# Performance work log

Measured on AMD Instinct MI355X. Metric: run time of the kernel, lower is better.

Reference implementation:

```python
import jax, jax.numpy as jnp
import numpy as np

DIM = 4096
N_HEADS = 32
HEAD_DIM = DIM // N_HEADS
BATCH = 2
SEQ = 1024
THETA = 10000.0
NEG_INF = -1e9


def _rope_cos_sin(seq_len, head_dim):
    # NOTE: original code constructs RotatePosEmbedding with config.dim but applies
    # it per-head; the only shape-consistent interpretation (standard Llama RoPE)
    # uses head_dim frequencies, which is what we implement.
    inv_freq = 1.0 / (THETA ** (jnp.arange(0, head_dim, 2, dtype=jnp.float32) / head_dim))
    angles = jnp.arange(seq_len, dtype=jnp.float32)[:, None] * inv_freq[None, :]  # [S, hd/2]
    return jnp.cos(angles), jnp.sin(angles)


def _apply_rope(x, cos, sin):
    # x: [B,S,H,hd]; rotate consecutive pairs (complex multiply)
    B, S, H, hd = x.shape
    xr = x.reshape(B, S, H, hd // 2, 2)
    x0, x1 = xr[..., 0], xr[..., 1]
    c = cos[None, :, None, :]
    s = sin[None, :, None, :]
    out = jnp.stack([x0 * c - x1 * s, x0 * s + x1 * c], axis=-1)
    return out.reshape(B, S, H, hd)


def setup_inputs() -> dict:
    key = jax.random.key(0)
    ks = jax.random.split(key, 9)
    x = jax.random.normal(ks[0], (BATCH, SEQ, DIM), dtype=jnp.float32)
    scale = 1.0 / np.sqrt(DIM)
    wq = jax.random.normal(ks[1], (DIM, DIM), dtype=jnp.float32) * scale
    wk = jax.random.normal(ks[2], (DIM, DIM), dtype=jnp.float32) * scale
    wv = jax.random.normal(ks[3], (DIM, DIM), dtype=jnp.float32) * scale
    wo = jax.random.normal(ks[4], (DIM, DIM), dtype=jnp.float32) * scale
    bq = jax.random.normal(ks[5], (DIM,), dtype=jnp.float32) * 0.01
    bk = jax.random.normal(ks[6], (DIM,), dtype=jnp.float32) * 0.01
    bv = jax.random.normal(ks[7], (DIM,), dtype=jnp.float32) * 0.01
    bo = jax.random.normal(ks[8], (DIM,), dtype=jnp.float32) * 0.01
    # causal additive mask [S,S]
    mask = jnp.where(jnp.tril(jnp.ones((SEQ, SEQ), dtype=bool)), 0.0, NEG_INF).astype(jnp.float32)
    return {"x": x, "wq": wq, "bq": bq, "wk": wk, "bk": bk, "wv": wv, "bv": bv,
            "wo": wo, "bo": bo, "mask": mask, "start_pos": 0}


def reference(x, wq, bq, wk, bk, wv, bv, wo, bo, mask, start_pos):
    B, S, D = x.shape
    H, hd = N_HEADS, D // N_HEADS
    q = (x @ wq.T + bq).reshape(B, S, H, hd)
    k = (x @ wk.T + bk).reshape(B, S, H, hd)
    v = (x @ wv.T + bv).reshape(B, S, H, hd)
    cos, sin = _rope_cos_sin(S, hd)
    q = _apply_rope(q, cos, sin)
    k = _apply_rope(k, cos, sin)
    # start_pos == 0 prefill: cache slice [:start_pos+S] equals current k/v
    scores = jnp.einsum('bqhd,bkhd->bhqk', q, k) / np.sqrt(hd).astype(np.float32)
    scores = scores + mask[None, None, :, :]
    attn = jax.nn.softmax(scores, axis=-1)
    out = jnp.einsum('bhqk,bkhd->bqhd', attn, v).reshape(B, S, D)
    return out @ wo.T + bo
```

## Files before the change

kernel.cpp:

```cpp
#include <hip/hip_runtime.h>
#include <hip/hip_bf16.h>

#define DIM   4096
#define NH    32
#define HD    128
#define BATCH 2
#define SEQ   1024
#define MROWS (BATCH*SEQ)
#define LDQ   12288

typedef __attribute__((ext_vector_type(8))) short bf16x8;
typedef __attribute__((ext_vector_type(4))) short s16x4;
typedef __attribute__((ext_vector_type(4))) float f32x4;

__device__ inline void gload_lds16(const void* g, void* l) {
  __builtin_amdgcn_global_load_lds(
      (const __attribute__((address_space(1))) void*)g,
      (__attribute__((address_space(3))) void*)l, 16, 0, 0);
}

__device__ inline float bf2f(short b) {
  unsigned u = ((unsigned)(unsigned short)b) << 16;
  return __uint_as_float(u);
}
__device__ inline unsigned short f2bfu(float f) {
  __hip_bfloat16 h = __float2bfloat16(f);
  return *reinterpret_cast<unsigned short*>(&h);
}

template <int N> __device__ __forceinline__ void wait_vm() {
  if constexpr (N == 0)      asm volatile("s_waitcnt vmcnt(0)" ::: "memory");
  else if constexpr (N == 7) asm volatile("s_waitcnt vmcnt(7)" ::: "memory");
  else                       asm volatile("s_waitcnt vmcnt(8)" ::: "memory");
}

__global__ void cvt_bf16_kernel(const float* __restrict__ in,
                                unsigned short* __restrict__ out, long n4) {
  long i = blockIdx.x * (long)blockDim.x + threadIdx.x;
  long stride = (long)gridDim.x * blockDim.x;
  for (; i < n4; i += stride) {
    float4 v = ((const float4*)in)[i];
    ushort4 o;
    o.x = f2bfu(v.x); o.y = f2bfu(v.y); o.z = f2bfu(v.z); o.w = f2bfu(v.w);
    ((ushort4*)out)[i] = o;
  }
}

__global__ void concat3_kernel(const float* __restrict__ a, const float* __restrict__ b,
                               const float* __restrict__ c, float* __restrict__ o) {
  int i = blockIdx.x * blockDim.x + threadIdx.x;
  if (i < 4096) o[i] = a[i];
  else if (i < 8192) o[i] = b[i - 4096];
  else if (i < 12288) o[i] = c[i - 8192];
}

__global__ void rope_table_kernel(float* __restrict__ cosT, float* __restrict__ sinT) {
  int s = blockIdx.x;
  int p = threadIdx.x;
  float inv = powf(10000.0f, -((float)(2 * p)) / 128.0f);
  float a = (float)s * inv;
  cosT[s * 64 + p] = cosf(a);
  sinT[s * 64 + p] = sinf(a);
}

__global__ void reduce_bias_kernel(const float* __restrict__ part,
                                   const float* __restrict__ bias,
                                   float* __restrict__ out) {
  long i = blockIdx.x * (long)blockDim.x + threadIdx.x;
  if (i >= (long)MROWS * DIM / 4) return;
  float4 a = ((const float4*)part)[i];
  float4 b = ((const float4*)(part + (size_t)MROWS * DIM))[i];
  float4 bb = ((const float4*)bias)[(int)(i & (DIM / 4 - 1))];
  float4 o;
  o.x = a.x + b.x + bb.x; o.y = a.y + b.y + bb.y;
  o.z = a.z + b.z + bb.z; o.w = a.w + b.w + bb.w;
  ((float4*)out)[i] = o;
}

template <typename OutT, bool QKV_MODE, int NB>
__global__ __launch_bounds__(512, 2) void gemm_q_kernel(
    const unsigned short* __restrict__ A, const unsigned short* __restrict__ Bw,
    const float* __restrict__ bias, OutT* __restrict__ C,
    int M, int N, int Kstr, int Klen,
    const float* __restrict__ cosT, const float* __restrict__ sinT) {
  constexpr int CBF = NB / 64;
  constexpr int BL  = NB / 64;
  constexpr int VM  = 4 + BL;
  constexpr int WNC = NB / 4;
  __shared__ unsigned short As[2][256 * 64];
  __shared__ unsigned short Bs[2][NB * 64];
  const int t = threadIdx.x;
  const int lane = t & 63;
  const int w = t >> 6;
  const int wm = w >> 2, wn = w & 3;
  const int np = lane & 15, hq = lane >> 4;

  int bid = blockIdx.y * gridDim.x + blockIdx.x;
  int nwg = gridDim.x * gridDim.y;
  int sb = (bid & 7) * (nwg >> 3) + (bid >> 3);
  int bx = sb % gridDim.x, by = sb / gridDim.x;
  const int m0 = by * 256, n0 = bx * NB;
  const int kb0 = blockIdx.z * Klen;
  const int NT = Klen >> 6;
  OutT* Cz = C + (size_t)blockIdx.z * M * N;

  auto stageA2 = [&](unsigned short* Asl, int kcol0, int j0) {
#pragma unroll
    for (int j = j0; j < j0 + 2; ++j) {
      int ci = j * 512 + t;
      int r = ci >> 3, c = ci & 7;
      gload_lds16(A + (size_t)(m0 + r) * Kstr + kcol0 + ((c ^ (r & 7)) << 3), Asl + ci * 8);
    }
  };
  auto stageB = [&](unsigned short* Bsl, int kcol0) {
#pragma unroll
    for (int j = 0; j < BL; ++j) {
      int ci = j * 512 + t;
      int r = ci >> 3, c = ci & 7;
      gload_lds16(Bw + (size_t)(n0 + r) * Kstr + kcol0 + ((c ^ (r & 7)) << 3), Bsl + ci * 8);
    }
  };

  stageA2(As[0], kb0, 0); stageA2(As[0], kb0, 2); stageB(Bs[0], kb0);
  stageA2(As[1], kb0 + 64, 0); stageA2(As[1], kb0 + 64, 2); stageB(Bs[1], kb0 + 64);

  f32x4 acc[8][CBF] = {};

  wait_vm<VM>();
  __builtin_amdgcn_s_barrier();

  int cur = 0;
#pragma unroll 1
  for (int kt = 0; kt < NT; ++kt) {
    const unsigned short* Asl = As[cur];
    const unsigned short* Bsl = Bs[cur];
    const int swz = np & 7;
    const int kn = kb0 + ((kt + 2) << 6);
    const bool more = (kt + 2 < NT);
    bf16x8 al[4][2], ah[4][2], bf[CBF][2];

#pragma unroll
    for (int rb = 0; rb < 4; ++rb)
#pragma unroll
      for (int kh = 0; kh < 2; ++kh)
        al[rb][kh] = *(const bf16x8*)&Asl[(wm * 128 + rb * 16 + np) * 64 +
                                          (((kh * 4 + hq) ^ swz) << 3)];
#pragma unroll
    for (int cb = 0; cb < CBF; ++cb)
#pragma unroll
      for (int kh = 0; kh < 2; ++kh)
        bf[cb][kh] = *(const bf16x8*)&Bsl[(wn * WNC + cb * 16 + np) * 64 +
                                          (((kh * 4 + hq) ^ swz) << 3)];
    __builtin_amdgcn_s_barrier();
    __builtin_amdgcn_s_setprio(1);
#pragma unroll
    for (int i = 0; i < 4; ++i)
#pragma unroll
      for (int j = 0; j < 2; ++j) {
        acc[i][j] = __builtin_amdgcn_mfma_f32_16x16x32_bf16(al[i][0], bf[j][0], acc[i][j], 0, 0, 0);
        acc[i][j] = __builtin_amdgcn_mfma_f32_16x16x32_bf16(al[i][1], bf[j][1], acc[i][j], 0, 0, 0);
      }
    __builtin_amdgcn_s_setprio(0);

#pragma unroll
    for (int rb = 0; rb < 4; ++rb)
#pragma unroll
      for (int kh = 0; kh < 2; ++kh)
        ah[rb][kh] = *(const bf16x8*)&Asl[(wm * 128 + 64 + rb * 16 + np) * 64 +
                                          (((kh * 4 + hq) ^ swz) << 3)];
    asm volatile("s_waitcnt lgkmcnt(0)" ::: "memory");
    __builtin_amdgcn_sched_barrier(0);
    __builtin_amdgcn_s_barrier();
    if (more) stageA2(As[cur], kn, 0);
    __builtin_amdgcn_s_setprio(1);
#pragma unroll
    for (int i = 0; i < 4; ++i)
#pragma unroll
      for (int j = 2; j < CBF; ++j) {
        acc[i][j] = __builtin_amdgcn_mfma_f32_16x16x32_bf16(al[i][0], bf[j][0], acc[i][j], 0, 0, 0);
        acc[i][j] = __builtin_amdgcn_mfma_f32_16x16x32_bf16(al[i][1], bf[j][1], acc[i][j], 0, 0, 0);
      }
    __builtin_amdgcn_s_setprio(0);
    __builtin_amdgcn_s_barrier();

    if (more) stageA2(As[cur], kn, 2);
    __builtin_amdgcn_s_setprio(1);
#pragma unroll
    for (int i = 0; i < 4; ++i)
#pragma unroll
      for (int j = 0; j < 2; ++j) {
        acc[i + 4][j] = __builtin_amdgcn_mfma_f32_16x16x32_bf16(ah[i][0], bf[j][0], acc[i + 4][j], 0, 0, 0);
        acc[i + 4][j] = __builtin_amdgcn_mfma_f32_16x16x32_bf16(ah[i][1], bf[j][1], acc[i + 4][j], 0, 0, 0);
      }
    __builtin_amdgcn_s_setprio(0);
    __builtin_amdgcn_s_barrier();

    if (more) stageB(Bs[cur], kn);
    __builtin_amdgcn_s_setprio(1);
#pragma unroll
    for (int i = 0; i < 4; ++i)
#pragma unroll
      for (int j = 2; j < CBF; ++j) {
        acc[i + 4][j] = __builtin_amdgcn_mfma_f32_16x16x32_bf16(ah[i][0], bf[j][0], acc[i + 4][j], 0, 0, 0);
        acc[i + 4][j] = __builtin_amdgcn_mfma_f32_16x16x32_bf16(ah[i][1], bf[j][1], acc[i + 4][j], 0, 0, 0);
      }
    __builtin_amdgcn_s_setprio(0);
    if (more) wait_vm<VM>();
    else      wait_vm<0>();
    __builtin_amdgcn_s_barrier();
    cur ^= 1;
  }

  const int orow0 = m0 + wm * 128;
  const int ocol0 = n0 + wn * WNC + np;
#pragma unroll
  for (int j = 0; j < CBF; ++j) {
    const int col = ocol0 + j * 16;
    float bj = QKV_MODE ? bias[col] : 0.0f;
    const int p0 = (col & 127) >> 1;
    const bool even = (lane & 1) == 0;
    const bool do_rope = QKV_MODE && (col < 8192);
#pragma unroll
    for (int i = 0; i < 8; ++i) {
#pragma unroll
      for (int r = 0; r < 4; ++r) {
        int orow = orow0 + i * 16 + hq * 4 + r;
        float v = acc[i][j][r] + bj;
        float pv = __shfl_xor(v, 1);
        if (do_rope) {
          int srow = orow & (SEQ - 1);
          float c = cosT[srow * 64 + p0];
          float s = sinT[srow * 64 + p0];
          v = even ? (v * c - pv * s) : (pv * s + v * c);
        }
        size_t off = (size_t)orow * N + col;
        if constexpr (sizeof(OutT) == 2)
          ((unsigned short*)Cz)[off] = f2bfu(v);
        else
          ((float*)Cz)[off] = v;
      }
    }
  }
}

__global__ __launch_bounds__(256, 1) void flash_attn_kernel(
    const unsigned short* __restrict__ QKV, unsigned short* __restrict__ O) {
  __shared__ unsigned short Ks[64 * 128];
  __shared__ unsigned short Vt[128 * 64];
  __shared__ unsigned short Ps[4][32 * 64];

  const int p  = blockIdx.x;
  const int bh = blockIdx.y;
  const int b  = bh >> 5;
  const int hh = bh & 31;
  const int t    = threadIdx.x;
  const int lane = t & 63;
  const int w    = t >> 6;
  const int np   = lane & 15;
  const int hq   = lane >> 4;

  const size_t rowbase = (size_t)b * SEQ * LDQ;
  const unsigned short* Qg = QKV + rowbase + (size_t)hh * HD;
  const unsigned short* Kg = QKV + rowbase + 4096 + (size_t)hh * HD;
  const unsigned short* Vg = QKV + rowbase + 8192 + (size_t)hh * HD;
  unsigned short* Og = O + (size_t)b * SEQ * DIM + (size_t)hh * HD;

  const int krow = t >> 2;
  const int kc0  = (t & 3) * 32;
  const int vr0  = (t & 15) * 4;
  const int vc0  = (t >> 4) * 8;

  unsigned short* Pw = &Ps[w][0];
  const float SCALE = 0.08838834764831843f;

  bf16x8 vk[4], vv[4];

#pragma unroll 1
  for (int pass = 0; pass < 2; ++pass) {
    const int qt    = pass ? (7 - p) : p;
    const int nt    = 2 * qt + 2;
    const int qbase = qt * 128 + w * 32;

    bf16x8 qf[2][4];
#pragma unroll
    for (int rb = 0; rb < 2; ++rb)
#pragma unroll
      for (int kb = 0; kb < 4; ++kb)
        qf[rb][kb] = *(const bf16x8*)&Qg[(size_t)(qbase + rb * 16 + np) * LDQ + kb * 32 + hq * 8];

    f32x4 acc[2][8] = {};
    float m_run[2][4], l_run[2][4];
#pragma unroll
    for (int rb = 0; rb < 2; ++rb)
#pragma unroll
      for (int r = 0; r < 4; ++r) { m_run[rb][r] = -3.0e38f; l_run[rb][r] = 0.0f; }

    {
      const unsigned short* kp = Kg + (size_t)krow * LDQ + kc0;
      const unsigned short* vp = Vg + (size_t)vr0 * LDQ + vc0;
#pragma unroll
      for (int jj = 0; jj < 4; ++jj) vk[jj] = *(const bf16x8*)(kp + jj * 8);
#pragma unroll
      for (int jj = 0; jj < 4; ++jj) vv[jj] = *(const bf16x8*)(vp + (size_t)jj * LDQ);
    }

#pragma unroll 1
    for (int kt = 0; kt < nt; ++kt) {
      __syncthreads();

#pragma unroll
      for (int jj = 0; jj < 4; ++jj) {
        int c = (t & 3) * 4 + jj;
        *(bf16x8*)((char*)Ks + krow * 256 + ((c ^ (krow & 7)) << 4)) = vk[jj];
      }
#pragma unroll
      for (int i = 0; i < 8; ++i) {
        int col = vc0 + i;
        s16x4 sv;
        sv[0] = vv[0][i]; sv[1] = vv[1][i]; sv[2] = vv[2][i]; sv[3] = vv[3][i];
        *(s16x4*)((char*)Vt + ((col * 128 + vr0 * 2) ^ ((col & 7) << 4))) = sv;
      }
      __syncthreads();

      if (kt + 1 < nt) {
        const unsigned short* kp = Kg + (size_t)((kt + 1) * 64 + krow) * LDQ + kc0;
        const unsigned short* vp = Vg + (size_t)((kt + 1) * 64 + vr0) * LDQ + vc0;
#pragma unroll
        for (int jj = 0; jj < 4; ++jj) vk[jj] = *(const bf16x8*)(kp + jj * 8);
#pragma unroll
        for (int jj = 0; jj < 4; ++jj) vv[jj] = *(const bf16x8*)(vp + (size_t)jj * LDQ);
      }

      f32x4 sc[4][2] = {};
#pragma unroll
      for (int ct = 0; ct < 4; ++ct) {
#pragma unroll
        for (int kb = 0; kb < 4; ++kb) {
          bf16x8 kf = *(const bf16x8*)((char*)Ks + (ct * 16 + np) * 256 +
                                       (((kb * 4 + hq) ^ (np & 7)) << 4));
          sc[ct][0] = __builtin_amdgcn_mfma_f32_16x16x32_bf16(qf[0][kb], kf, sc[ct][0], 0, 0, 0);
          sc[ct][1] = __builtin_amdgcn_mfma_f32_16x16x32_bf16(qf[1][kb], kf, sc[ct][1], 0, 0, 0);
        }
      }

      const bool maskt = (kt >= 2 * qt);
#pragma unroll
      for (int ct = 0; ct < 4; ++ct) {
        int kvc = kt * 64 + ct * 16 + np;
#pragma unroll
        for (int rb = 0; rb < 2; ++rb)
#pragma unroll
          for (int r = 0; r < 4; ++r) {
            float v = sc[ct][rb][r] * SCALE;
            if (maskt && kvc > qbase + rb * 16 + hq * 4 + r) v = -1.0e9f;
            sc[ct][rb][r] = v;
          }
      }

      float sf[2][4];
#pragma unroll
      for (int rb = 0; rb < 2; ++rb)
#pragma unroll
        for (int r = 0; r < 4; ++r) {
          float tmax = fmaxf(fmaxf(sc[0][rb][r], sc[1][rb][r]),
                             fmaxf(sc[2][rb][r], sc[3][rb][r]));
          tmax = fmaxf(tmax, __shfl_xor(tmax, 1));
          tmax = fmaxf(tmax, __shfl_xor(tmax, 2));
          tmax = fmaxf(tmax, __shfl_xor(tmax, 4));
          tmax = fmaxf(tmax, __shfl_xor(tmax, 8));
          float mn = fmaxf(m_run[rb][r], tmax);
          sf[rb][r] = __expf(m_run[rb][r] - mn);
          m_run[rb][r] = mn;
        }

#pragma unroll
      for (int rb = 0; rb < 2; ++rb)
#pragma unroll
        for (int r = 0; r < 4; ++r) {
          int prow = rb * 16 + hq * 4 + r;
          int swz = (prow & 7) << 4;
          float rsum = 0.f;
#pragma unroll
          for (int ct = 0; ct < 4; ++ct) {
            float pv = __expf(sc[ct][rb][r] - m_run[rb][r]);
            rsum += pv;
            *(unsigned short*)((char*)Pw + ((prow * 128 + (ct * 16 + np) * 2) ^ swz)) = f2bfu(pv);
          }
          rsum += __shfl_xor(rsum, 1);
          rsum += __shfl_xor(rsum, 2);
          rsum += __shfl_xor(rsum, 4);
          rsum += __shfl_xor(rsum, 8);
          l_run[rb][r] = l_run[rb][r] * sf[rb][r] + rsum;
        }

#pragma unroll
      for (int rb = 0; rb < 2; ++rb)
#pragma unroll
        for (int nt2 = 0; nt2 < 8; ++nt2)
#pragma unroll
          for (int r = 0; r < 4; ++r)
            acc[rb][nt2][r] *= sf[rb][r];

#pragma unroll
      for (int kb2 = 0; kb2 < 2; ++kb2) {
        bf16x8 pa0 = *(const bf16x8*)((char*)Pw +
            (((0 * 16 + np) * 128 + kb2 * 64 + hq * 16) ^ ((np & 7) << 4)));
        bf16x8 pa1 = *(const bf16x8*)((char*)Pw +
            (((1 * 16 + np) * 128 + kb2 * 64 + hq * 16) ^ ((np & 7) << 4)));
#pragma unroll
        for (int nt2 = 0; nt2 < 8; ++nt2) {
          int col = nt2 * 16 + np;
          bf16x8 vf = *(const bf16x8*)((char*)Vt +
              ((col * 128 + kb2 * 64 + hq * 16) ^ ((col & 7) << 4)));
          acc[0][nt2] = __builtin_amdgcn_mfma_f32_16x16x32_bf16(pa0, vf, acc[0][nt2], 0, 0, 0);
          acc[1][nt2] = __builtin_amdgcn_mfma_f32_16x16x32_bf16(pa1, vf, acc[1][nt2], 0, 0, 0);
        }
      }
    }

#pragma unroll
    for (int rb = 0; rb < 2; ++rb)
#pragma unroll
      for (int r = 0; r < 4; ++r) {
        float rl = 1.0f / l_run[rb][r];
        int orow = qbase + rb * 16 + hq * 4 + r;
#pragma unroll
        for (int nt2 = 0; nt2 < 8; ++nt2)
          Og[(size_t)orow * DIM + nt2 * 16 + np] = f2bfu(acc[rb][nt2][r] * rl);
      }
  }
}

extern "C" void kernel_launch(void* const* d_in, const int* in_sizes, int n_in,
                              void* d_out, int out_size, void* d_ws, size_t ws_size,
                              hipStream_t stream) {
  const float* x  = (const float*)d_in[0];
  const float* wq = (const float*)d_in[1];
  const float* bq = (const float*)d_in[2];
  const float* wk = (const float*)d_in[3];
  const float* bk = (const float*)d_in[4];
  const float* wv = (const float*)d_in[5];
  const float* bv = (const float*)d_in[6];
  const float* wo = (const float*)d_in[7];
  const float* bo = (const float*)d_in[8];
  float* out = (float*)d_out;

  char* ws = (char*)d_ws;
  unsigned short* wqkvb = (unsigned short*)(ws);
  float* part           = (float*)(ws);
  unsigned short* wob   = (unsigned short*)(ws + (96ll  << 20));
  unsigned short* xb    = (unsigned short*)(ws + (128ll << 20));
  unsigned short* qkv   = (unsigned short*)(ws + (144ll << 20));
  unsigned short* ab    = (unsigned short*)(ws + (192ll << 20));
  float* biasqkv = (float*)(ws + (208ll << 20));
  float* cosT    = (float*)(ws + (208ll << 20) + (64  << 10));
  float* sinT    = (float*)(ws + (208ll << 20) + (320 << 10));

  cvt_bf16_kernel<<<2048, 256, 0, stream>>>(x,  xb, (long)MROWS * DIM / 4);
  cvt_bf16_kernel<<<2048, 256, 0, stream>>>(wq, wqkvb,                        (long)DIM * DIM / 4);
  cvt_bf16_kernel<<<2048, 256, 0, stream>>>(wk, wqkvb + (size_t)DIM * DIM,    (long)DIM * DIM / 4);
  cvt_bf16_kernel<<<2048, 256, 0, stream>>>(wv, wqkvb + 2 * (size_t)DIM * DIM,(long)DIM * DIM / 4);
  cvt_bf16_kernel<<<2048, 256, 0, stream>>>(wo, wob, (long)DIM * DIM / 4);

  concat3_kernel<<<48, 256, 0, stream>>>(bq, bk, bv, biasqkv);
  rope_table_kernel<<<SEQ, 64, 0, stream>>>(cosT, sinT);

  dim3 gq(LDQ / 192, MROWS / 256, 1);
  gemm_q_kernel<unsigned short, true, 192><<<gq, 512, 0, stream>>>(
      xb, wqkvb, biasqkv, qkv, MROWS, LDQ, DIM, DIM, cosT, sinT);

  dim3 ga(4, BATCH * NH);
  flash_attn_kernel<<<ga, 256, 0, stream>>>(qkv, ab);

  dim3 go(DIM / 256, MROWS / 256, 2);
  gemm_q_kernel<float, false, 256><<<go, 512, 0, stream>>>(
      ab, wob, nullptr, part, MROWS, DIM, DIM, DIM / 2, nullptr, nullptr);

  reduce_bias_kernel<<<(MROWS * DIM / 4 + 255) / 256, 256, 0, stream>>>(part, bo, out);
}
```

Baseline: 529.2 us.

## Rewrite GEMM as 4-stage K=32 pipeline with fixed 256x256 tiles

Replaces the double-buffered K=64 GEMM, which interleaved partial stage loads between MFMA chunks under several barriers, with a four-slot ring of K=32 LDS buffers. Loads run three tiles ahead and each iteration needs only one barrier. The QKV GEMM now uses 256-wide N tiles instead of 192, giving 48x8 blocks. The aim is to cut barrier count and hide global-load latency better, at the cost of more iterations, a new swizzle, and fewer QKV workgroups.

```diff
diff --git a/kernel.cpp b/kernel.cpp
--- a/kernel.cpp
+++ b/kernel.cpp
@@ -30,7 +30,7 @@
 
 template <int N> __device__ __forceinline__ void wait_vm() {
   if constexpr (N == 0)      asm volatile("s_waitcnt vmcnt(0)" ::: "memory");
-  else if constexpr (N == 7) asm volatile("s_waitcnt vmcnt(7)" ::: "memory");
+  else if constexpr (N == 4) asm volatile("s_waitcnt vmcnt(4)" ::: "memory");
   else                       asm volatile("s_waitcnt vmcnt(8)" ::: "memory");
 }
 
@@ -77,18 +77,14 @@
   ((float4*)out)[i] = o;
 }
 
-template <typename OutT, bool QKV_MODE, int NB>
-__global__ __launch_bounds__(512, 2) void gemm_q_kernel(
+template <typename OutT, bool QKV_MODE>
+__global__ __launch_bounds__(512, 2) void gemm_v3_kernel(
     const unsigned short* __restrict__ A, const unsigned short* __restrict__ Bw,
     const float* __restrict__ bias, OutT* __restrict__ C,
     int M, int N, int Kstr, int Klen,
     const float* __restrict__ cosT, const float* __restrict__ sinT) {
-  constexpr int CBF = NB / 64;
-  constexpr int BL  = NB / 64;
-  constexpr int VM  = 4 + BL;
-  constexpr int WNC = NB / 4;
-  __shared__ unsigned short As[2][256 * 64];
-  __shared__ unsigned short Bs[2][NB * 64];
+  __shared__ unsigned short As[4][256 * 32];
+  __shared__ unsigned short Bs[4][256 * 32];
   const int t = threadIdx.x;
   const int lane = t & 63;
   const int w = t >> 6;
@@ -99,122 +95,77 @@
   int nwg = gridDim.x * gridDim.y;
   int sb = (bid & 7) * (nwg >> 3) + (bid >> 3);
   int bx = sb % gridDim.x, by = sb / gridDim.x;
-  const int m0 = by * 256, n0 = bx * NB;
+  const int m0 = by * 256, n0 = bx * 256;
   const int kb0 = blockIdx.z * Klen;
-  const int NT = Klen >> 6;
-  OutT* Cz = C + (size_t)blockIdx.z * M * N;
-
-  auto stageA2 = [&](unsigned short* Asl, int kcol0, int j0) {
-#pragma unroll
-    for (int j = j0; j < j0 + 2; ++j) {
+  const int NT = Klen >> 5;
+  OutT* Cz = C + (size_t)blockIdx.z * (size_t)M * N;
+
+  auto stage = [&](int slot, int kcol0) {
+#pragma unroll
+    for (int j = 0; j < 2; ++j) {
       int ci = j * 512 + t;
-      int r = ci >> 3, c = ci & 7;
-      gload_lds16(A + (size_t)(m0 + r) * Kstr + kcol0 + ((c ^ (r & 7)) << 3), Asl + ci * 8);
+      int r = ci >> 2, cg = (ci & 3) ^ ((r >> 1) & 3);
+      gload_lds16(A + (size_t)(m0 + r) * Kstr + kcol0 + cg * 8, &As[slot][ci * 8]);
+    }
+#pragma unroll
+    for (int j = 0; j < 2; ++j) {
+      int ci = j * 512 + t;
+      int r = ci >> 2, cg = (ci & 3) ^ ((r >> 1) & 3);
+      gload_lds16(Bw + (size_t)(n0 + r) * Kstr + kcol0 + cg * 8, &Bs[slot][ci * 8]);
     }
   };
-  auto stageB = [&](unsigned short* Bsl, int kcol0) {
-#pragma unroll
-    for (int j = 0; j < BL; ++j) {
-      int ci = j * 512 + t;
-      int r = ci >> 3, c = ci & 7;
-      gload_lds16(Bw + (size_t)(n0 + r) * Kstr + kcol0 + ((c ^ (r & 7)) << 3), Bsl + ci * 8);
-    }
-  };
-
-  stageA2(As[0], kb0, 0); stageA2(As[0], kb0, 2); stageB(Bs[0], kb0);
-  stageA2(As[1], kb0 + 64, 0); stageA2(As[1], kb0 + 64, 2); stageB(Bs[1], kb0 + 64);
-
-  f32x4 acc[8][CBF] = {};
-
-  wait_vm<VM>();
+
+  stage(0, kb0); stage(1, kb0 + 32); stage(2, kb0 + 64);
+
+  f32x4 acc[8][4] = {};
+
+  wait_vm<8>();
   __builtin_amdgcn_s_barrier();
 
-  int cur = 0;
 #pragma unroll 1
-  for (int kt = 0; kt < NT; ++kt) {
-    const unsigned short* Asl = As[cur];
-    const unsigned short* Bsl = Bs[cur];
-    const int swz = np & 7;
-    const int kn = kb0 + ((kt + 2) << 6);
-    const bool more = (kt + 2 < NT);
-    bf16x8 al[4][2], ah[4][2], bf[CBF][2];
-
-#pragma unroll
-    for (int rb = 0; rb < 4; ++rb)
-#pragma unroll
-      for (int kh = 0; kh < 2; ++kh)
-        al[rb][kh] = *(const bf16x8*)&Asl[(wm * 128 + rb * 16 + np) * 64 +
-                                          (((kh * 4 + hq) ^ swz) << 3)];
-#pragma unroll
-    for (int cb = 0; cb < CBF; ++cb)
-#pragma unroll
-      for (int kh = 0; kh < 2; ++kh)
-        bf[cb][kh] = *(const bf16x8*)&Bsl[(wn * WNC + cb * 16 + np) * 64 +
-                                          (((kh * 4 + hq) ^ swz) << 3)];
+  for (int u = 0; u < NT; ++u) {
+    const unsigned short* Asl = As[u & 3];
+    const unsigned short* Bsl = Bs[u & 3];
+    const int cswz = (np >> 1) & 3;
+    const int kc = (hq ^ cswz) << 3;
+    bf16x8 af[8], bf[4];
+#pragma unroll
+    for (int i = 0; i < 4; ++i)
+      af[i] = *(const bf16x8*)&Asl[(wm * 128 + i * 16 + np) * 32 + kc];
+#pragma unroll
+    for (int j = 0; j < 4; ++j)
+      bf[j] = *(const bf16x8*)&Bsl[(wn * 64 + j * 16 + np) * 32 + kc];
+#pragma unroll
+    for (int i = 4; i < 8; ++i)
+      af[i] = *(const bf16x8*)&Asl[(wm * 128 + i * 16 + np) * 32 + kc];
+
+    if (u + 3 < NT) stage((u + 3) & 3, kb0 + ((u + 3) << 5));
+
+    __builtin_amdgcn_s_setprio(1);
+#pragma unroll
+    for (int i = 0; i < 4; ++i)
+#pragma unroll
+      for (int j = 0; j < 4; ++j)
+        acc[i][j] = __builtin_amdgcn_mfma_f32_16x16x32_bf16(af[i], bf[j], acc[i][j], 0, 0, 0);
+    __builtin_amdgcn_s_setprio(0);
+    __builtin_amdgcn_s_setprio(1);
+#pragma unroll
+    for (int i = 4; i < 8; ++i)
+#pragma unroll
+      for (int j = 0; j < 4; ++j)
+        acc[i][j] = __builtin_amdgcn_mfma_f32_16x16x32_bf16(af[i], bf[j], acc[i][j], 0, 0, 0);
+    __builtin_amdgcn_s_setprio(0);
+
+    if (u + 3 < NT)      wait_vm<8>();
+    else if (u + 2 < NT) wait_vm<4>();
+    else                 wait_vm<0>();
     __builtin_amdgcn_s_barrier();
-    __builtin_amdgcn_s_setprio(1);
-#pragma unroll
-    for (int i = 0; i < 4; ++i)
-#pragma unroll
-      for (int j = 0; j < 2; ++j) {
-        acc[i][j] = __builtin_amdgcn_mfma_f32_16x16x32_bf16(al[i][0], bf[j][0], acc[i][j], 0, 0, 0);
-        acc[i][j] = __builtin_amdgcn_mfma_f32_16x16x32_bf16(al[i][1], bf[j][1], acc[i][j], 0, 0, 0);
-      }
-    __builtin_amdgcn_s_setprio(0);
-
-#pragma unroll
-    for (int rb = 0; rb < 4; ++rb)
-#pragma unroll
-      for (int kh = 0; kh < 2; ++kh)
-        ah[rb][kh] = *(const bf16x8*)&Asl[(wm * 128 + 64 + rb * 16 + np) * 64 +
-                                          (((kh * 4 + hq) ^ swz) << 3)];
-    asm volatile("s_waitcnt lgkmcnt(0)" ::: "memory");
-    __builtin_amdgcn_sched_barrier(0);
-    __builtin_amdgcn_s_barrier();
-    if (more) stageA2(As[cur], kn, 0);
-    __builtin_amdgcn_s_setprio(1);
-#pragma unroll
-    for (int i = 0; i < 4; ++i)
-#pragma unroll
-      for (int j = 2; j < CBF; ++j) {
-        acc[i][j] = __builtin_amdgcn_mfma_f32_16x16x32_bf16(al[i][0], bf[j][0], acc[i][j], 0, 0, 0);
-        acc[i][j] = __builtin_amdgcn_mfma_f32_16x16x32_bf16(al[i][1], bf[j][1], acc[i][j], 0, 0, 0);
-      }
-    __builtin_amdgcn_s_setprio(0);
-    __builtin_amdgcn_s_barrier();
-
-    if (more) stageA2(As[cur], kn, 2);
-    __builtin_amdgcn_s_setprio(1);
-#pragma unroll
-    for (int i = 0; i < 4; ++i)
-#pragma unroll
-      for (int j = 0; j < 2; ++j) {
-        acc[i + 4][j] = __builtin_amdgcn_mfma_f32_16x16x32_bf16(ah[i][0], bf[j][0], acc[i + 4][j], 0, 0, 0);
-        acc[i + 4][j] = __builtin_amdgcn_mfma_f32_16x16x32_bf16(ah[i][1], bf[j][1], acc[i + 4][j], 0, 0, 0);
-      }
-    __builtin_amdgcn_s_setprio(0);
-    __builtin_amdgcn_s_barrier();
-
-    if (more) stageB(Bs[cur], kn);
-    __builtin_amdgcn_s_setprio(1);
-#pragma unroll
-    for (int i = 0; i < 4; ++i)
-#pragma unroll
-      for (int j = 2; j < CBF; ++j) {
-        acc[i + 4][j] = __builtin_amdgcn_mfma_f32_16x16x32_bf16(ah[i][0], bf[j][0], acc[i + 4][j], 0, 0, 0);
-        acc[i + 4][j] = __builtin_amdgcn_mfma_f32_16x16x32_bf16(ah[i][1], bf[j][1], acc[i + 4][j], 0, 0, 0);
-      }
-    __builtin_amdgcn_s_setprio(0);
-    if (more) wait_vm<VM>();
-    else      wait_vm<0>();
-    __builtin_amdgcn_s_barrier();
-    cur ^= 1;
   }
 
   const int orow0 = m0 + wm * 128;
-  const int ocol0 = n0 + wn * WNC + np;
-#pragma unroll
-  for (int j = 0; j < CBF; ++j) {
+  const int ocol0 = n0 + wn * 64 + np;
+#pragma unroll
+  for (int j = 0; j < 4; ++j) {
     const int col = ocol0 + j * 16;
     float bj = QKV_MODE ? bias[col] : 0.0f;
     const int p0 = (col & 127) >> 1;
@@ -465,15 +416,15 @@
   concat3_kernel<<<48, 256, 0, stream>>>(bq, bk, bv, biasqkv);
   rope_table_kernel<<<SEQ, 64, 0, stream>>>(cosT, sinT);
 
-  dim3 gq(LDQ / 192, MROWS / 256, 1);
-  gemm_q_kernel<unsigned short, true, 192><<<gq, 512, 0, stream>>>(
+  dim3 gq(LDQ / 256, MROWS / 256, 1);
+  gemm_v3_kernel<unsigned short, true><<<gq, 512, 0, stream>>>(
       xb, wqkvb, biasqkv, qkv, MROWS, LDQ, DIM, DIM, cosT, sinT);
 
   dim3 ga(4, BATCH * NH);
   flash_attn_kernel<<<ga, 256, 0, stream>>>(qkv, ab);
 
   dim3 go(DIM / 256, MROWS / 256, 2);
-  gemm_q_kernel<float, false, 256><<<go, 512, 0, stream>>>(
+  gemm_v3_kernel<float, false><<<go, 512, 0, stream>>>(
       ab, wob, nullptr, part, MROWS, DIM, DIM, DIM / 2, nullptr, nullptr);
 
   reduce_bias_kernel<<<(MROWS * DIM / 4 + 255) / 256, 256, 0, stream>>>(part, bo, out);
```

Measured after the change: 533.6 us. Within noise of the previous version (+0.8%).
